# Performance work log

Hardware: AMD Instinct MI355X
Metric: run time of the kernel (lower is better)

## Reference

```python
import jax, jax.numpy as jnp
import numpy as np

HIDDEN = 768
HEADS = 12
HEAD_DIM = 64
SEQ = 512
DS_K = 64  # downsampling_k
EPS = 1e-6


def setup_inputs() -> dict:
    key = jax.random.key(0)
    ks = jax.random.split(key, 16)
    B = 32
    sd = 1.0 / DS_K
    glorot = jax.nn.initializers.lecun_normal()  # flax default_kernel_init
    inp = {
        "query": jax.random.normal(ks[0], (B, SEQ, HIDDEN), jnp.float32),
        "key": jax.random.normal(ks[1], (B, SEQ, HIDDEN), jnp.float32),
        "value": jax.random.normal(ks[2], (B, SEQ, HIDDEN), jnp.float32),
        "step": 0,
        # learned Linformer-style downsampling projections [k, s]
        "W_kds": sd * jax.random.normal(ks[3], (DS_K, SEQ), jnp.float32),
        "W_vds": sd * jax.random.normal(ks[4], (DS_K, SEQ), jnp.float32),
        # DenseGeneral qkv kernels [d, n, h] and biases [n, h]
        "Wq": glorot(ks[5], (HIDDEN, HEADS, HEAD_DIM), jnp.float32),
        "bq": jnp.zeros((HEADS, HEAD_DIM), jnp.float32),
        "Wk": glorot(ks[6], (HIDDEN, HEADS, HEAD_DIM), jnp.float32),
        "bk": jnp.zeros((HEADS, HEAD_DIM), jnp.float32),
        "Wv": glorot(ks[7], (HIDDEN, HEADS, HEAD_DIM), jnp.float32),
        "bv": jnp.zeros((HEADS, HEAD_DIM), jnp.float32),
        # out projection contracts (n, h) -> hidden
        "Wout": glorot(ks[8], (HEADS * HEAD_DIM, HIDDEN), jnp.float32).reshape(HEADS, HEAD_DIM, HIDDEN),
        "bout": jnp.zeros((HIDDEN,), jnp.float32),
    }
    return inp


def reference(query, key, value, step, W_kds, W_vds, Wq, bq, Wk, bk, Wv, bv, Wout, bout):
    # Linformer-style downsample of keys/values along sequence: [b,s,d] -> [b,k,d]
    key_ds = jnp.einsum("ks,bsd->bkd", W_kds, key)
    val_ds = jnp.einsum("ks,bsd->bkd", W_vds, value)

    # per-head projections
    queries = jnp.einsum("bqd,dnh->bqnh", query, Wq) + bq    # [b,q,n,h]
    keys = jnp.einsum("bkd,dnh->bknh", key_ds, Wk) + bk      # [b,k,n,h]
    values = jnp.einsum("bkd,dnh->bknh", val_ds, Wv) + bv    # [b,k,n,h]

    # kernelized linear attention with elu feature map (mask=False path)
    phi_q = jax.nn.elu(queries) + 1.0
    phi_k = jax.nn.elu(keys) + 1.0
    s = jnp.einsum("bknd,bknh->bndh", phi_k, values)          # [b,n,h,h] KV state
    z = jnp.sum(phi_k, axis=1)                                 # [b,n,h]
    qs = jnp.einsum("bqnd,bndh->bqnh", phi_q, s)
    qz = jnp.einsum("bqnd,bnd->bqn", phi_q, z) + EPS
    a_v = qs / qz[..., None]                                   # [b,q,n,h]

    out = jnp.einsum("bqnh,nhD->bqD", a_v, Wout) + bout        # [b,q,hidden]
    return out
```

## Files before the change

kernel.cpp:

```cpp
#include <hip/hip_runtime.h>

typedef unsigned short u16;
typedef u16 u16x4 __attribute__((ext_vector_type(4)));
typedef u16 u16x8 __attribute__((ext_vector_type(8)));
typedef __bf16 bf16;
typedef bf16 bf16x8 __attribute__((ext_vector_type(8)));
typedef float f32x4 __attribute__((ext_vector_type(4)));

__device__ __forceinline__ float bf2f(u16 v) {
  union { unsigned u; float f; } x; x.u = ((unsigned)v) << 16; return x.f;
}
__device__ __forceinline__ u16 f2bf(float f) {
  union { float f; unsigned u; } x; x.f = f;
  unsigned u = x.u;
  u += 0x7fffu + ((u >> 16) & 1u);
  return (u16)(u >> 16);
}

#define GLDS16(g, l) __builtin_amdgcn_global_load_lds( \
    (const __attribute__((address_space(1))) unsigned int*)(const void*)(g), \
    (__attribute__((address_space(3))) unsigned int*)(void*)(l), 16, 0, 0)

__global__ __launch_bounds__(256) void prepds_k(
    const float* __restrict__ Wq, const float* __restrict__ Wk,
    const float* __restrict__ Wv, const float* __restrict__ Wout,
    const float* __restrict__ query,
    const float* __restrict__ W_kds, const float* __restrict__ W_vds,
    const float* __restrict__ b0, const float* __restrict__ b1,
    const float* __restrict__ b2, const float* __restrict__ b3,
    const float* __restrict__ key, const float* __restrict__ value,
    u16* __restrict__ WT, u16* __restrict__ q_bf,
    u16* __restrict__ dstB, u16* __restrict__ key_ds)
{
  __shared__ char sm[50176];
  const int blk = blockIdx.x;
  const int t = threadIdx.x;

  if (blk % 10 == 0) {
    const int id = blk / 10;
    float* Sg = (float*)sm;
    u16* Wbf = (u16*)(sm + 32768);
    const int nt = (id % 12) * 64;
    const int yb = id / 12;
    const int pair = yb >> 5, b = yb & 31;
    const float* src = (pair ? value : key) + (size_t)b * 512 * 768;
    const float* W32 = pair ? W_vds : W_kds;
    u16* dst = key_ds + (size_t)pair * 1572864 + (size_t)b * 49152;
    const int wave = t >> 6, lane = t & 63;
    const int wm = (wave >> 1) * 32, wn = (wave & 1) * 32;
    const int lrow = lane & 15, quad = lane >> 4;
    const int gr = lane >> 4;
    const int gc = (lane & 15) * 16;
    const int wrow = t >> 5;
    const int wcol = (t & 31) * 4;
    f32x4 acc[2][2] = {};

    for (int ph = 0; ph < 4; ++ph) {
      const int kb = ph * 128;
      #pragma unroll
      for (int j = 0; j < 8; ++j) {
        const int idx = wave * 8 + j;
        const float* gsrc = src + (size_t)(kb + idx * 4 + gr) * 768 + nt;
        GLDS16((const char*)gsrc + gc, (char*)Sg + idx * 1024);
      }
      f32x4 wr[8];
      #pragma unroll
      for (int i = 0; i < 8; ++i)
        wr[i] = *(const f32x4*)&W32[(size_t)(i * 8 + wrow) * 512 + kb + wcol];
      #pragma unroll
      for (int i = 0; i < 8; ++i) {
        u16x4 wv4;
        #pragma unroll
        for (int q2 = 0; q2 < 4; ++q2) wv4[q2] = f2bf(wr[i][q2]);
        *(u16x4*)&Wbf[(i * 8 + wrow) * 136 + wcol] = wv4;
      }
      __syncthreads();
      #pragma unroll
      for (int s = 0; s < 4; ++s) {
        bf16x8 av[2], bv[2];
        #pragma unroll
        for (int i = 0; i < 2; ++i)
          av[i] = *(const bf16x8*)&Wbf[(wm + i * 16 + lrow) * 136 + s * 32 + quad * 8];
        #pragma unroll
        for (int j = 0; j < 2; ++j) {
          const int n2 = wn + j * 16 + lrow;
          u16x8 bb;
          #pragma unroll
          for (int e = 0; e < 8; ++e) bb[e] = f2bf(Sg[(s * 32 + quad * 8 + e) * 64 + n2]);
          bv[j] = *(bf16x8*)&bb;
        }
        #pragma unroll
        for (int i = 0; i < 2; ++i)
          #pragma unroll
          for (int j = 0; j < 2; ++j)
            acc[i][j] = __builtin_amdgcn_mfma_f32_16x16x32_bf16(av[i], bv[j], acc[i][j], 0, 0, 0);
      }
      __syncthreads();
    }
    #pragma unroll
    for (int i = 0; i < 2; ++i)
      #pragma unroll
      for (int j = 0; j < 2; ++j) {
        const int col = nt + wn + j * 16 + lrow;
        #pragma unroll
        for (int r = 0; r < 4; ++r) {
          const int row = wm + i * 16 + quad * 4 + r;
          dst[(size_t)row * 768 + col] = f2bf(acc[i][j][r]);
        }
      }
    return;
  }

  const int pid = blk - blk / 10 - 1;
  if (pid < 576) {
    u16 (*T)[72] = (u16(*)[72])sm;
    const int bz = pid / 144, rr = pid % 144;
    const int r0 = (rr / 12) * 64, c0 = (rr % 12) * 64;
    const float* W = (bz == 0) ? Wq : (bz == 1) ? Wk : (bz == 2) ? Wv : Wout;
    u16* O = WT + (size_t)bz * 768 * 768;
    #pragma unroll
    for (int p = 0; p < 2; ++p) {
      int v = t + p * 256;
      int r = v / 8, c = (v % 8) * 8;
      f32x4 x0 = *(const f32x4*)&W[(size_t)(r0 + r) * 768 + c0 + c];
      f32x4 x1 = *(const f32x4*)&W[(size_t)(r0 + r) * 768 + c0 + c + 4];
      #pragma unroll
      for (int i = 0; i < 4; ++i) { T[r][c + i] = f2bf(x0[i]); T[r][c + 4 + i] = f2bf(x1[i]); }
    }
    __syncthreads();
    #pragma unroll
    for (int p = 0; p < 2; ++p) {
      int v = t + p * 256;
      int r = v / 8, c = (v % 8) * 8;
      u16x8 tv;
      #pragma unroll
      for (int i = 0; i < 8; ++i) tv[i] = T[c + i][r];
      *(u16x8*)&O[(size_t)(c0 + r) * 768 + r0 + c] = tv;
    }
  } else if (pid < 6720) {
    const size_t i = (size_t)(pid - 576) * 256 + t;
    f32x4 a = *(const f32x4*)&query[i * 8];
    f32x4 b = *(const f32x4*)&query[i * 8 + 4];
    u16x8 w;
    #pragma unroll
    for (int j = 0; j < 4; ++j) { w[j] = f2bf(a[j]); w[4 + j] = f2bf(b[j]); }
    *(u16x8*)&q_bf[i * 8] = w;
  } else if (pid < 6732) {
    const int i = (pid - 6720) * 256 + t;
    if (i < 3072) {
      int s = i / 768, si = i % 768;
      const float* src = (s == 0) ? b0 : (s == 1) ? b1 : (s == 2) ? b2 : b3;
      dstB[i] = f2bf(src[si]);
    }
  }
}

__global__ __launch_bounds__(256) void fkv_k(
    const u16* __restrict__ key_ds,
    const u16* __restrict__ WT,
    const u16* __restrict__ bias_c,
    u16* __restrict__ sT, float* __restrict__ z)
{
  __shared__ char sm[32768];
  u16* T0 = (u16*)sm;
  u16* Pt = (u16*)sm;
  u16* Vt = (u16*)(sm + 9216);
  const int x = blockIdx.x;
  const int b = x / 12, n = x % 12;
  const int t = threadIdx.x, wave = t >> 6, lane = t & 63;
  const u16* srcs[4] = {
    key_ds + (size_t)b * 49152,
    WT + 589824 + (size_t)n * 49152,
    key_ds + 1572864 + (size_t)b * 49152,
    WT + 2 * 589824 + (size_t)n * 49152 };
  const int grow = lane >> 3;
  const int gchunk = (lane & 7) ^ (grow & 7);
  const int isV = wave & 1;
  const int wm = (wave >> 1) * 32;
  const u16* Atile_s = srcs[isV ? 2 : 0];
  (void)Atile_s;
  const u16* Asrc = srcs[isV ? 2 : 0];
  const u16* Bsrc = srcs[isV ? 3 : 1];
  (void)Asrc; (void)Bsrc;
  u16* Atile = T0 + (isV ? 2 : 0) * 4096;
  u16* Btile = T0 + (isV ? 3 : 1) * 4096;
  const int lrow = lane & 15, quad = lane >> 4;
  f32x4 acc[2][4] = {};

  for (int k0 = 0; k0 < 768; k0 += 64) {
    const u16* s = srcs[wave];
    u16* dtile = T0 + wave * 4096;
    #pragma unroll
    for (int j = 0; j < 8; ++j) {
      const u16* gsrc = s + (size_t)(j * 8 + grow) * 768 + k0 + gchunk * 8;
      GLDS16(gsrc, (char*)dtile + j * 1024);
    }
    __syncthreads();
    #pragma unroll
    for (int c = 0; c < 2; ++c) {
      bf16x8 av[2], bv[4];
      #pragma unroll
      for (int i = 0; i < 2; ++i) {
        const int row = wm + i * 16 + lrow;
        av[i] = *(const bf16x8*)&Atile[row * 64 + (((c * 4 + quad) ^ (row & 7)) * 8)];
      }
      #pragma unroll
      for (int j = 0; j < 4; ++j) {
        const int row = j * 16 + lrow;
        bv[j] = *(const bf16x8*)&Btile[row * 64 + (((c * 4 + quad) ^ (row & 7)) * 8)];
      }
      #pragma unroll
      for (int i = 0; i < 2; ++i)
        #pragma unroll
        for (int j = 0; j < 4; ++j)
          acc[i][j] = __builtin_amdgcn_mfma_f32_16x16x32_bf16(av[i], bv[j], acc[i][j], 0, 0, 0);
    }
    __syncthreads();
  }

  const u16* bias = bias_c + (isV ? 1536 : 768) + n * 64;
  u16* Ttile = isV ? Vt : Pt;
  #pragma unroll
  for (int i = 0; i < 2; ++i)
    #pragma unroll
    for (int j = 0; j < 4; ++j) {
      const int col = j * 16 + lrow;
      const float badd = bf2f(bias[col]);
      u16x4 pk4;
      #pragma unroll
      for (int r = 0; r < 4; ++r) {
        float v = acc[i][j][r] + badd;
        if (!isV) v = v > 0.0f ? v + 1.0f : __expf(v);
        pk4[r] = f2bf(v);
      }
      *(u16x4*)&Ttile[col * 72 + wm + i * 16 + quad * 4] = pk4;
    }
  __syncthreads();

  const int wm2 = (wave >> 1) * 32, wn2 = (wave & 1) * 32;
  f32x4 a2[2][2] = {};
  #pragma unroll
  for (int c = 0; c < 2; ++c) {
    bf16x8 av[2], bv[2];
    #pragma unroll
    for (int i = 0; i < 2; ++i)
      av[i] = *(const bf16x8*)&Vt[(wm2 + i * 16 + lrow) * 72 + c * 32 + quad * 8];
    #pragma unroll
    for (int j = 0; j < 2; ++j)
      bv[j] = *(const bf16x8*)&Pt[(wn2 + j * 16 + lrow) * 72 + c * 32 + quad * 8];
    #pragma unroll
    for (int i = 0; i < 2; ++i)
      #pragma unroll
      for (int j = 0; j < 2; ++j)
        a2[i][j] = __builtin_amdgcn_mfma_f32_16x16x32_bf16(av[i], bv[j], a2[i][j], 0, 0, 0);
  }
  u16* sTg = sT + (size_t)x * 4096;
  #pragma unroll
  for (int i = 0; i < 2; ++i)
    #pragma unroll
    for (int j = 0; j < 2; ++j)
      #pragma unroll
      for (int r = 0; r < 4; ++r)
        sTg[(size_t)(wm2 + i * 16 + quad * 4 + r) * 64 + wn2 + j * 16 + lrow] = f2bf(a2[i][j][r]);
  if (t < 64) {
    float zz = 0.f;
    #pragma unroll
    for (int g = 0; g < 8; ++g) {
      u16x8 p = *(const u16x8*)&Pt[t * 72 + g * 8];
      #pragma unroll
      for (int e = 0; e < 8; ++e) zz += bf2f(p[e]);
    }
    z[(size_t)x * 64 + t] = zz;
  }
}

template<int ACT, bool OF32>
__global__ __launch_bounds__(256) void gemm97_k(
    const u16* __restrict__ A, int lda,
    const u16* __restrict__ Bt, int ldb,
    void* __restrict__ Craw, int ldc,
    const u16* __restrict__ bias, int K)
{
  __shared__ u16 As[128 * 32];
  __shared__ u16 Bs[128 * 32];
  const int mt = blockIdx.x * 128, nt = blockIdx.y * 128;
  const int t = threadIdx.x, wave = t >> 6, lane = t & 63;
  const int wm = (wave >> 1) * 64, wn = (wave & 1) * 64;
  const int lrow = lane & 15, quad = lane >> 4;
  f32x4 acc[4][4] = {};

  for (int k0 = 0; k0 < K; k0 += 32) {
    __syncthreads();
    #pragma unroll
    for (int p = 0; p < 2; ++p) {
      const int s = wave * 128 + p * 64 + lane;
      const int r = s >> 2, c = (s & 3) * 8;
      const int lb = (wave * 128 + p * 64) * 8;
      GLDS16(&A[(size_t)(mt + r) * lda + k0 + c], &As[lb]);
      GLDS16(&Bt[(size_t)(nt + r) * ldb + k0 + c], &Bs[lb]);
    }
    __syncthreads();

    bf16x8 av[4], bv[4];
    #pragma unroll
    for (int i = 0; i < 4; ++i) av[i] = *(const bf16x8*)&As[(wm + i * 16 + lrow) * 32 + quad * 8];
    #pragma unroll
    for (int j = 0; j < 4; ++j) bv[j] = *(const bf16x8*)&Bs[(wn + j * 16 + lrow) * 32 + quad * 8];
    #pragma unroll
    for (int i = 0; i < 4; ++i)
      #pragma unroll
      for (int j = 0; j < 4; ++j)
        acc[i][j] = __builtin_amdgcn_mfma_f32_16x16x32_bf16(av[i], bv[j], acc[i][j], 0, 0, 0);
  }

  #pragma unroll
  for (int i = 0; i < 4; ++i) {
    #pragma unroll
    for (int j = 0; j < 4; ++j) {
      const int col = nt + wn + j * 16 + lrow;
      const float badd = bias ? bf2f(bias[col]) : 0.0f;
      #pragma unroll
      for (int r = 0; r < 4; ++r) {
        const int row = mt + wm + i * 16 + quad * 4 + r;
        float v = acc[i][j][r] + badd;
        if constexpr (ACT == 1) v = v > 0.0f ? v + 1.0f : __expf(v);
        if constexpr (OF32) ((float*)Craw)[(size_t)row * ldc + col] = v;
        else                ((u16*)Craw)[(size_t)row * ldc + col] = f2bf(v);
      }
    }
  }
}

__global__ __launch_bounds__(256) void attn_av_k(
    u16* __restrict__ phi_q, const u16* __restrict__ sT, const float* __restrict__ zbuf)
{
  __shared__ u16 As[64 * 72];
  __shared__ u16 Bs[64 * 72];
  __shared__ float zv[64];
  __shared__ float zpart[4][64];
  __shared__ float zq[64];
  const int x = blockIdx.x, y = blockIdx.y;
  const int b = y / 12, n = y % 12;
  const int t = threadIdx.x;
  u16* Abase = phi_q + (size_t)b * 512 * 768 + (size_t)x * 64 * 768 + n * 64;
  const u16* Bbase = sT + (size_t)y * 4096;
  if (t < 64) zv[t] = zbuf[(size_t)y * 64 + t];
  #pragma unroll
  for (int p = 0; p < 2; ++p) {
    int v = t + p * 256;
    int r = v >> 3, c = (v & 7) * 8;
    *(u16x8*)&As[r * 72 + c] = *(const u16x8*)&Abase[(size_t)r * 768 + c];
    *(u16x8*)&Bs[r * 72 + c] = *(const u16x8*)&Bbase[r * 64 + c];
  }
  __syncthreads();
  {
    int r = t & 63, seg = t >> 6;
    float s = 0.f;
    #pragma unroll
    for (int j = 0; j < 16; ++j) s += bf2f(As[r * 72 + seg * 16 + j]) * zv[seg * 16 + j];
    zpart[seg][r] = s;
  }
  __syncthreads();
  if (t < 64) {
    float s = zpart[0][t] + zpart[1][t] + zpart[2][t] + zpart[3][t];
    zq[t] = 1.0f / (s + 1e-6f);
  }
  const int wave = t >> 6, lane = t & 63;
  const int wm = (wave >> 1) * 32, wn = (wave & 1) * 32;
  const int lrow = lane & 15, quad = lane >> 4;
  f32x4 acc[2][2] = {};
  #pragma unroll
  for (int c = 0; c < 2; ++c) {
    bf16x8 av[2], bv[2];
    #pragma unroll
    for (int i = 0; i < 2; ++i) av[i] = *(const bf16x8*)&As[(wm + i * 16 + lrow) * 72 + c * 32 + quad * 8];
    #pragma unroll
    for (int j = 0; j < 2; ++j) bv[j] = *(const bf16x8*)&Bs[(wn + j * 16 + lrow) * 72 + c * 32 + quad * 8];
    #pragma unroll
    for (int i = 0; i < 2; ++i)
      #pragma unroll
      for (int j = 0; j < 2; ++j)
        acc[i][j] = __builtin_amdgcn_mfma_f32_16x16x32_bf16(av[i], bv[j], acc[i][j], 0, 0, 0);
  }
  __syncthreads();
  #pragma unroll
  for (int i = 0; i < 2; ++i)
    #pragma unroll
    for (int j = 0; j < 2; ++j) {
      const int col = wn + j * 16 + lrow;
      #pragma unroll
      for (int r = 0; r < 4; ++r) {
        const int row = wm + i * 16 + quad * 4 + r;
        Abase[(size_t)row * 768 + col] = f2bf(acc[i][j][r] * zq[row]);
      }
    }
}

__global__ void tagfill_k(float* out, float val, int n) {
  int i = blockIdx.x * 256 + threadIdx.x;
  if (i < n) out[i] = val;
}

extern "C" void kernel_launch(void* const* d_in, const int* in_sizes, int n_in,
                              void* d_out, int out_size, void* d_ws, size_t ws_size,
                              hipStream_t stream) {
  (void)out_size;
  float* out = (float*)d_out;

  int o;
  if (n_in >= 14 && in_sizes[3] == 1) o = 4;
  else if (n_in == 13) o = 3;
  else { tagfill_k<<<4, 256, 0, stream>>>(out, 77.0f, 1024); return; }
  if (in_sizes[0] != 12582912 || in_sizes[o + 0] != 32768 || in_sizes[o + 2] != 589824) {
    tagfill_k<<<4, 256, 0, stream>>>(out, 88.0f, 1024); return;
  }

  const float* query = (const float*)d_in[0];
  const float* key   = (const float*)d_in[1];
  const float* value = (const float*)d_in[2];
  const float* W_kds = (const float*)d_in[o + 0];
  const float* W_vds = (const float*)d_in[o + 1];
  const float* Wq   = (const float*)d_in[o + 2];
  const float* bq   = (const float*)d_in[o + 3];
  const float* Wk   = (const float*)d_in[o + 4];
  const float* bk   = (const float*)d_in[o + 5];
  const float* Wv   = (const float*)d_in[o + 6];
  const float* bv   = (const float*)d_in[o + 7];
  const float* Wout = (const float*)d_in[o + 8];
  const float* bout = (const float*)d_in[o + 9];

  const size_t NEED = 61478912;
  if (ws_size < NEED) { tagfill_k<<<4, 256, 0, stream>>>(out, 123.0f, 1024); return; }

  char* base = (char*)d_ws;
  u16*   WT     = (u16*)base;
  char*  Breg   = base + 4718592;
  u16*   q_bf   = (u16*)Breg;
  u16*   sT     = (u16*)Breg;
  float* zbuf   = (float*)(Breg + 3145728);
  u16*   phi_q  = (u16*)(base + 29884416);
  u16*   bias_c = (u16*)(base + 55181312);
  u16*   key_ds = (u16*)(base + 55187456);
  u16* a_v = phi_q;
  u16* WqT   = WT;
  u16* WoutT = WT + 3 * 768 * 768;
  u16* bq_c = bias_c, *bout_c = bias_c + 2304;

  prepds_k<<<7680, 256, 0, stream>>>(Wq, Wk, Wv, Wout, query, W_kds, W_vds,
                                     bq, bk, bv, bout, key, value,
                                     WT, q_bf, bias_c, key_ds);

  gemm97_k<1, false><<<dim3(128, 6), 256, 0, stream>>>(
      q_bf, 768, WqT, 768, phi_q, 768, bq_c, 768);

  fkv_k<<<384, 256, 0, stream>>>(key_ds, WT, bias_c, sT, zbuf);

  attn_av_k<<<dim3(8, 384), 256, 0, stream>>>(phi_q, sT, zbuf);

  gemm97_k<0, true><<<dim3(128, 6), 256, 0, stream>>>(
      a_v, 768, WoutT, 768, out, 768, bout_c, 768);
}
```

Measured before the change: 318.2 us.

## Split key/value downsampling into a separate FP32 register-blocked kernel

The Linformer downsampling GEMM no longer sits inside the fused prep kernel, where it ran as bf16 MFMA blocks on every tenth block. It now runs in its own kernel, ds_k, which uses FP32 FMA with register blocking: each thread owns 2 columns and 16 output rows and double-buffers the streamed key/value rows. The aim is to stream the 100 MB of fp32 key/value input at closer to bandwidth, without LDS staging and without per-element bf16 conversion of the source. The costs are an extra kernel launch, a grid of only 768 blocks of 128 threads, and every source row being read 4 times, once per z-slice, which may mostly hit in cache. Some dead code in fkv_k is also removed.

```diff
diff --git a/kernel.cpp b/kernel.cpp
--- a/kernel.cpp
+++ b/kernel.cpp
@@ -5,6 +5,7 @@
 typedef u16 u16x8 __attribute__((ext_vector_type(8)));
 typedef __bf16 bf16;
 typedef bf16 bf16x8 __attribute__((ext_vector_type(8)));
+typedef float f32x2 __attribute__((ext_vector_type(2)));
 typedef float f32x4 __attribute__((ext_vector_type(4)));
 
 __device__ __forceinline__ float bf2f(u16 v) {
@@ -21,100 +22,19 @@
     (const __attribute__((address_space(1))) unsigned int*)(const void*)(g), \
     (__attribute__((address_space(3))) unsigned int*)(void*)(l), 16, 0, 0)
 
-__global__ __launch_bounds__(256) void prepds_k(
+__global__ __launch_bounds__(256) void prep_k(
     const float* __restrict__ Wq, const float* __restrict__ Wk,
     const float* __restrict__ Wv, const float* __restrict__ Wout,
     const float* __restrict__ query,
-    const float* __restrict__ W_kds, const float* __restrict__ W_vds,
     const float* __restrict__ b0, const float* __restrict__ b1,
     const float* __restrict__ b2, const float* __restrict__ b3,
-    const float* __restrict__ key, const float* __restrict__ value,
-    u16* __restrict__ WT, u16* __restrict__ q_bf,
-    u16* __restrict__ dstB, u16* __restrict__ key_ds)
+    u16* __restrict__ WT, u16* __restrict__ q_bf, u16* __restrict__ dstB)
 {
-  __shared__ char sm[50176];
+  __shared__ u16 T[64][72];
   const int blk = blockIdx.x;
   const int t = threadIdx.x;
-
-  if (blk % 10 == 0) {
-    const int id = blk / 10;
-    float* Sg = (float*)sm;
-    u16* Wbf = (u16*)(sm + 32768);
-    const int nt = (id % 12) * 64;
-    const int yb = id / 12;
-    const int pair = yb >> 5, b = yb & 31;
-    const float* src = (pair ? value : key) + (size_t)b * 512 * 768;
-    const float* W32 = pair ? W_vds : W_kds;
-    u16* dst = key_ds + (size_t)pair * 1572864 + (size_t)b * 49152;
-    const int wave = t >> 6, lane = t & 63;
-    const int wm = (wave >> 1) * 32, wn = (wave & 1) * 32;
-    const int lrow = lane & 15, quad = lane >> 4;
-    const int gr = lane >> 4;
-    const int gc = (lane & 15) * 16;
-    const int wrow = t >> 5;
-    const int wcol = (t & 31) * 4;
-    f32x4 acc[2][2] = {};
-
-    for (int ph = 0; ph < 4; ++ph) {
-      const int kb = ph * 128;
-      #pragma unroll
-      for (int j = 0; j < 8; ++j) {
-        const int idx = wave * 8 + j;
-        const float* gsrc = src + (size_t)(kb + idx * 4 + gr) * 768 + nt;
-        GLDS16((const char*)gsrc + gc, (char*)Sg + idx * 1024);
-      }
-      f32x4 wr[8];
-      #pragma unroll
-      for (int i = 0; i < 8; ++i)
-        wr[i] = *(const f32x4*)&W32[(size_t)(i * 8 + wrow) * 512 + kb + wcol];
-      #pragma unroll
-      for (int i = 0; i < 8; ++i) {
-        u16x4 wv4;
-        #pragma unroll
-        for (int q2 = 0; q2 < 4; ++q2) wv4[q2] = f2bf(wr[i][q2]);
-        *(u16x4*)&Wbf[(i * 8 + wrow) * 136 + wcol] = wv4;
-      }
-      __syncthreads();
-      #pragma unroll
-      for (int s = 0; s < 4; ++s) {
-        bf16x8 av[2], bv[2];
-        #pragma unroll
-        for (int i = 0; i < 2; ++i)
-          av[i] = *(const bf16x8*)&Wbf[(wm + i * 16 + lrow) * 136 + s * 32 + quad * 8];
-        #pragma unroll
-        for (int j = 0; j < 2; ++j) {
-          const int n2 = wn + j * 16 + lrow;
-          u16x8 bb;
-          #pragma unroll
-          for (int e = 0; e < 8; ++e) bb[e] = f2bf(Sg[(s * 32 + quad * 8 + e) * 64 + n2]);
-          bv[j] = *(bf16x8*)&bb;
-        }
-        #pragma unroll
-        for (int i = 0; i < 2; ++i)
-          #pragma unroll
-          for (int j = 0; j < 2; ++j)
-            acc[i][j] = __builtin_amdgcn_mfma_f32_16x16x32_bf16(av[i], bv[j], acc[i][j], 0, 0, 0);
-      }
-      __syncthreads();
-    }
-    #pragma unroll
-    for (int i = 0; i < 2; ++i)
-      #pragma unroll
-      for (int j = 0; j < 2; ++j) {
-        const int col = nt + wn + j * 16 + lrow;
-        #pragma unroll
-        for (int r = 0; r < 4; ++r) {
-          const int row = wm + i * 16 + quad * 4 + r;
-          dst[(size_t)row * 768 + col] = f2bf(acc[i][j][r]);
-        }
-      }
-    return;
-  }
-
-  const int pid = blk - blk / 10 - 1;
-  if (pid < 576) {
-    u16 (*T)[72] = (u16(*)[72])sm;
-    const int bz = pid / 144, rr = pid % 144;
+  if (blk < 576) {
+    const int bz = blk / 144, rr = blk % 144;
     const int r0 = (rr / 12) * 64, c0 = (rr % 12) * 64;
     const float* W = (bz == 0) ? Wq : (bz == 1) ? Wk : (bz == 2) ? Wv : Wout;
     u16* O = WT + (size_t)bz * 768 * 768;
@@ -137,21 +57,77 @@
       for (int i = 0; i < 8; ++i) tv[i] = T[c + i][r];
       *(u16x8*)&O[(size_t)(c0 + r) * 768 + r0 + c] = tv;
     }
-  } else if (pid < 6720) {
-    const size_t i = (size_t)(pid - 576) * 256 + t;
+  } else if (blk < 6720) {
+    const size_t i = (size_t)(blk - 576) * 256 + t;
     f32x4 a = *(const f32x4*)&query[i * 8];
     f32x4 b = *(const f32x4*)&query[i * 8 + 4];
     u16x8 w;
     #pragma unroll
     for (int j = 0; j < 4; ++j) { w[j] = f2bf(a[j]); w[4 + j] = f2bf(b[j]); }
     *(u16x8*)&q_bf[i * 8] = w;
-  } else if (pid < 6732) {
-    const int i = (pid - 6720) * 256 + t;
+  } else {
+    const int i = (blk - 6720) * 256 + t;
     if (i < 3072) {
       int s = i / 768, si = i % 768;
       const float* src = (s == 0) ? b0 : (s == 1) ? b1 : (s == 2) ? b2 : b3;
       dstB[i] = f2bf(src[si]);
     }
+  }
+}
+
+__global__ __launch_bounds__(128) void ds_k(
+    const float* __restrict__ W_kds, const float* __restrict__ W_vds,
+    const float* __restrict__ key, const float* __restrict__ value,
+    u16* __restrict__ key_ds)
+{
+  const int t = threadIdx.x;
+  const int pair = blockIdx.y >> 5, b = blockIdx.y & 31;
+  const float* src = (pair ? value : key) + (size_t)b * 512 * 768
+                   + blockIdx.x * 256 + t * 2;
+  const float* W32 = (pair ? W_vds : W_kds) + (size_t)blockIdx.z * 16 * 512;
+  u16* dst = key_ds + (size_t)pair * 1572864 + (size_t)b * 49152
+           + (size_t)blockIdx.z * 16 * 768 + blockIdx.x * 256 + t * 2;
+
+  f32x2 acc[16] = {};
+  f32x2 xa[8], xb[8];
+  #pragma unroll
+  for (int u = 0; u < 8; ++u) xa[u] = *(const f32x2*)&src[(size_t)u * 768];
+
+  #pragma unroll 1
+  for (int s0 = 0; s0 < 496; s0 += 16) {
+    #pragma unroll
+    for (int u = 0; u < 8; ++u) xb[u] = *(const f32x2*)&src[(size_t)(s0 + 8 + u) * 768];
+    #pragma unroll
+    for (int u = 0; u < 8; ++u) {
+      #pragma unroll
+      for (int m = 0; m < 16; ++m) acc[m] += xa[u] * W32[m * 512 + s0 + u];
+    }
+    #pragma unroll
+    for (int u = 0; u < 8; ++u) xa[u] = *(const f32x2*)&src[(size_t)(s0 + 16 + u) * 768];
+    #pragma unroll
+    for (int u = 0; u < 8; ++u) {
+      #pragma unroll
+      for (int m = 0; m < 16; ++m) acc[m] += xb[u] * W32[m * 512 + s0 + 8 + u];
+    }
+  }
+  #pragma unroll
+  for (int u = 0; u < 8; ++u) xb[u] = *(const f32x2*)&src[(size_t)(504 + u) * 768];
+  #pragma unroll
+  for (int u = 0; u < 8; ++u) {
+    #pragma unroll
+    for (int m = 0; m < 16; ++m) acc[m] += xa[u] * W32[m * 512 + 496 + u];
+  }
+  #pragma unroll
+  for (int u = 0; u < 8; ++u) {
+    #pragma unroll
+    for (int m = 0; m < 16; ++m) acc[m] += xb[u] * W32[m * 512 + 504 + u];
+  }
+
+  #pragma unroll
+  for (int m = 0; m < 16; ++m) {
+    union { u16 h[2]; unsigned w; } o;
+    o.h[0] = f2bf(acc[m][0]); o.h[1] = f2bf(acc[m][1]);
+    *(unsigned*)&dst[(size_t)m * 768] = o.w;
   }
 }
 
@@ -177,11 +153,6 @@
   const int gchunk = (lane & 7) ^ (grow & 7);
   const int isV = wave & 1;
   const int wm = (wave >> 1) * 32;
-  const u16* Atile_s = srcs[isV ? 2 : 0];
-  (void)Atile_s;
-  const u16* Asrc = srcs[isV ? 2 : 0];
-  const u16* Bsrc = srcs[isV ? 3 : 1];
-  (void)Asrc; (void)Bsrc;
   u16* Atile = T0 + (isV ? 2 : 0) * 4096;
   u16* Btile = T0 + (isV ? 3 : 1) * 4096;
   const int lrow = lane & 15, quad = lane >> 4;
@@ -446,13 +417,14 @@
   u16* WoutT = WT + 3 * 768 * 768;
   u16* bq_c = bias_c, *bout_c = bias_c + 2304;
 
-  prepds_k<<<7680, 256, 0, stream>>>(Wq, Wk, Wv, Wout, query, W_kds, W_vds,
-                                     bq, bk, bv, bout, key, value,
-                                     WT, q_bf, bias_c, key_ds);
+  prep_k<<<6732, 256, 0, stream>>>(Wq, Wk, Wv, Wout, query,
+                                   bq, bk, bv, bout, WT, q_bf, bias_c);
 
   gemm97_k<1, false><<<dim3(128, 6), 256, 0, stream>>>(
       q_bf, 768, WqT, 768, phi_q, 768, bq_c, 768);
 
+  ds_k<<<dim3(3, 64, 4), 128, 0, stream>>>(W_kds, W_vds, key, value, key_ds);
+
   fkv_k<<<384, 256, 0, stream>>>(key_ds, WT, bias_c, sT, zbuf);
 
   attn_av_k<<<dim3(8, 384), 256, 0, stream>>>(phi_q, sT, zbuf);
```

Result: slower. 380.9 us (+19.7%).
